# Performance work log

Hardware: AMD Instinct MI355X
Metric: run time of the kernel (lower is better)

## Reference

```python
import jax, jax.numpy as jnp
import numpy as np

B, T, D, H = 4, 2048, 1024, 16
DH = D // H
T2 = T // 2
LN_EPS = 1e-5


def setup_inputs() -> dict:
    key = jax.random.key(0)
    ks = jax.random.split(key, 10)
    x = jax.random.normal(ks[0], (B, T, D), dtype=jnp.float32)
    query = jax.random.normal(ks[1], (1, 1, D), dtype=jnp.float32) * 0.02
    s = 1.0 / np.sqrt(D)
    Wk = jax.random.uniform(ks[2], (D, D), jnp.float32, -s, s)
    Wv = jax.random.uniform(ks[3], (D, D), jnp.float32, -s, s)
    Wt = jax.random.uniform(ks[4], (D, D // 2), jnp.float32, -s, s)
    bt = jax.random.uniform(ks[5], (D // 2,), jnp.float32, -s, s)
    Wm = jax.random.uniform(ks[6], (D, 1), jnp.float32, -s, s)
    bm = jax.random.uniform(ks[7], (1,), jnp.float32, -s, s)
    ln_g = jnp.ones((D,), jnp.float32)
    ln_b = jnp.zeros((D,), jnp.float32)
    return {"x": x, "query": query, "Wk": Wk, "Wv": Wv, "Wt": Wt,
            "bt": bt, "Wm": Wm, "bm": bm, "ln_g": ln_g, "ln_b": ln_b}


def reference(x, query, Wk, Wv, Wt, bt, Wm, bm, ln_g, ln_b):
    Bx, Tx, d = x.shape
    t2 = Tx // 2
    h, dh = H, DH
    # projections -> (B, T, H, dh)
    k = (x @ Wk).reshape(Bx, Tx, h, dh)
    v = (x @ Wv).reshape(Bx, Tx, h, dh)
    q = query.reshape(h, dh)  # single learned query, shared over all coarse positions
    # scores: (B, H, T) then broadcast to (B, H, T2, T) with position-dependent mask t > 2j
    scores = jnp.einsum('hd,bthd->bht', q, k) / jnp.sqrt(jnp.asarray(dh, x.dtype))
    j_idx = jnp.arange(t2)[:, None]   # (T2, 1)
    t_idx = jnp.arange(Tx)[None, :]   # (1, T)
    mask_bias = jnp.where(t_idx > 2 * j_idx, -jnp.inf, 0.0).astype(x.dtype)  # (T2, T)
    attn = jax.nn.softmax(scores[:, :, None, :] + mask_bias[None, None], axis=-1)  # (B,H,T2,T)
    pooled = jnp.einsum('bhjt,bthd->bjhd', attn, v).reshape(Bx, t2, d)  # (B, T2, d)
    # LayerNorm over last dim
    mu = jnp.mean(pooled, axis=-1, keepdims=True)
    var = jnp.mean(jnp.square(pooled - mu), axis=-1, keepdims=True)
    pooled_n = (pooled - mu) * jax.lax.rsqrt(var + LN_EPS) * ln_g + ln_b
    theta = pooled_n @ Wt + bt                 # (B, T2, d//2)
    mag = jax.nn.sigmoid(pooled_n @ Wm + bm)   # (B, T2, 1)
    return theta, mag
```

## Files before the change

kernel.cpp:

```cpp
#include <hip/hip_runtime.h>
#include <hip/hip_bf16.h>
#include <cstdint>
#include <cstddef>

constexpr int Bc  = 4;
constexpr int Tc  = 2048;
constexpr int Dc  = 1024;
constexpr int Hc  = 16;
constexpr int DHc = 64;
constexpr int T2c = 1024;
constexpr int NCc = 32;
constexpr int NEXT = 1152;
#define LN_EPS_F 1e-5f

typedef __attribute__((ext_vector_type(8))) short bf16x8;
typedef __attribute__((ext_vector_type(8))) ushort ushort8_t;
typedef __attribute__((ext_vector_type(4))) float f32x4;

__device__ inline ushort f2bf(float f) {
    union { float f; uint32_t u; } v; v.f = f;
    uint32_t r = v.u + 0x7FFFu + ((v.u >> 16) & 1u);
    return (ushort)(r >> 16);
}
__device__ inline float bf2f(ushort u) {
    union { uint32_t u; float f; } v; v.u = ((uint32_t)u) << 16;
    return v.f;
}

__device__ inline void store_out(float v, float* p)  { *p = v; }
__device__ inline void store_out(float v, ushort* p) { *p = f2bf(v); }

__device__ inline void async_copy16(const void* g, void* lds) {
    __builtin_amdgcn_global_load_lds(
        (const __attribute__((address_space(1))) void*)g,
        (__attribute__((address_space(3))) void*)lds, 16, 0, 0);
}

constexpr int PREP_CVT  = 8192;
constexpr int PREP_WV   = PREP_CVT + 1024;
constexpr int PREP_WT   = PREP_WV + 512;
constexpr int PREP_QK   = PREP_WT + 64;
constexpr int PREP_ZERO = PREP_QK + 56;

__global__ __launch_bounds__(256) void k_prep(const float* __restrict__ x,
                                              const float* __restrict__ Wv,
                                              const float* __restrict__ Wt,
                                              const float* __restrict__ Wk,
                                              const float* __restrict__ query,
                                              ushort* __restrict__ xb,
                                              ushort* __restrict__ WvXT,
                                              ushort* __restrict__ WtT) {
    __shared__ float tile[32][33];
    int blk = blockIdx.x;
    int tid = threadIdx.x;
    if (blk < PREP_CVT) {
        int i = (blk * 256 + tid) * 4;
        float4 f = *(const float4*)(x + i);
        ushort4 o;
        o.x = f2bf(f.x); o.y = f2bf(f.y); o.z = f2bf(f.z); o.w = f2bf(f.w);
        *(ushort4*)(xb + i) = o;
    } else if (blk < PREP_WV) {
        int b2 = blk - PREP_CVT;
        int bx = b2 & 31, by = b2 >> 5;
        int tx = tid & 31, ty = tid >> 5;
        #pragma unroll
        for (int r = 0; r < 32; r += 8)
            tile[ty + r][tx] = Wv[(size_t)(by * 32 + ty + r) * Dc + bx * 32 + tx];
        __syncthreads();
        #pragma unroll
        for (int r = 0; r < 32; r += 8)
            WvXT[(size_t)(bx * 32 + ty + r) * Dc + by * 32 + tx] = f2bf(tile[tx][ty + r]);
    } else if (blk < PREP_WT) {
        int b2 = blk - PREP_WV;
        int bx = b2 & 15, by = b2 >> 4;
        int tx = tid & 31, ty = tid >> 5;
        #pragma unroll
        for (int r = 0; r < 32; r += 8)
            tile[ty + r][tx] = Wt[(size_t)(by * 32 + ty + r) * (Dc / 2) + bx * 32 + tx];
        __syncthreads();
        #pragma unroll
        for (int r = 0; r < 32; r += 8)
            WtT[(size_t)(bx * 32 + ty + r) * Dc + by * 32 + tx] = f2bf(tile[tx][ty + r]);
    } else if (blk < PREP_QK) {
        int idx = (blk - PREP_WT) * 256 + tid;
        int h = idx >> 10, i = idx & (Dc - 1);
        const float* wrow = Wk + (size_t)i * Dc + h * DHc;
        const float* qh   = query + h * DHc;
        float s = 0.f;
        #pragma unroll 8
        for (int d = 0; d < DHc; ++d) s += wrow[d] * qh[d];
        WvXT[(size_t)(Dc + h) * Dc + i] = f2bf(s * 0.125f);
    } else {
        int idx = (blk - PREP_QK) * 256 + tid;
        uint4 z = {0, 0, 0, 0};
        *(uint4*)(WvXT + (size_t)1040 * Dc + idx * 8) = z;
    }
}

__global__ __launch_bounds__(256) void k_gemm_v(const ushort* __restrict__ A,
                                                const ushort* __restrict__ Bt,
                                                ushort* __restrict__ v,
                                                float* __restrict__ scores) {
    constexpr int K = Dc;
    __shared__ ushort As[128 * 32];
    __shared__ ushort Bs[128 * 32];
    int tid = threadIdx.x;
    int wid = tid >> 6, lane = tid & 63;
    int tile_m = blockIdx.x * 128, tile_n = blockIdx.y * 128;
    int wm = wid >> 1, wn = wid & 1;

    f32x4 acc[4][4] = {};

    int lrow = lane >> 2;
    int lchunk = lane & 3;
    int quad = lane >> 4, l15 = lane & 15;

    for (int k0 = 0; k0 < K; k0 += 32) {
        #pragma unroll
        for (int r = 0; r < 2; ++r) {
            int rowgrp = wid * 2 + r;
            int row = rowgrp * 16 + lrow;
            async_copy16(A + (size_t)(tile_m + row) * K + k0 + lchunk * 8,
                         &As[rowgrp * 16 * 32]);
        }
        #pragma unroll
        for (int r = 0; r < 2; ++r) {
            int rowgrp = wid * 2 + r;
            int row = rowgrp * 16 + lrow;
            async_copy16(Bt + (size_t)(tile_n + row) * K + k0 + lchunk * 8,
                         &Bs[rowgrp * 16 * 32]);
        }
        __syncthreads();

        bf16x8 a_frag[4], b_frag[4];
        #pragma unroll
        for (int i = 0; i < 4; ++i)
            a_frag[i] = *(const bf16x8*)&As[(wm * 64 + i * 16 + l15) * 32 + quad * 8];
        #pragma unroll
        for (int j = 0; j < 4; ++j)
            b_frag[j] = *(const bf16x8*)&Bs[(wn * 64 + j * 16 + l15) * 32 + quad * 8];
        #pragma unroll
        for (int i = 0; i < 4; ++i)
            #pragma unroll
            for (int j = 0; j < 4; ++j)
                acc[i][j] = __builtin_amdgcn_mfma_f32_16x16x32_bf16(
                    a_frag[i], b_frag[j], acc[i][j], 0, 0, 0);
        __syncthreads();
    }

    #pragma unroll
    for (int j = 0; j < 4; ++j) {
        int col = tile_n + wn * 64 + j * 16 + l15;
        #pragma unroll
        for (int i = 0; i < 4; ++i) {
            #pragma unroll
            for (int r = 0; r < 4; ++r) {
                int row = tile_m + wm * 64 + i * 16 + quad * 4 + r;
                float val = acc[i][j][r];
                if (col < Dc) {
                    v[(size_t)row * Dc + col] = f2bf(val);
                } else if (col < Dc + Hc) {
                    int h = col - Dc;
                    int b = row >> 11, t = row & (Tc - 1);
                    scores[((size_t)b * Hc + h) * Tc + t] = val;
                }
            }
        }
    }
}

template <bool BIAS, typename OutT>
__global__ __launch_bounds__(256) void k_gemm_bf16(const ushort* __restrict__ A,
                                                   const ushort* __restrict__ Bt,
                                                   const float* __restrict__ bias,
                                                   OutT* __restrict__ C,
                                                   int M, int N, int K) {
    __shared__ ushort As[128 * 32];
    __shared__ ushort Bs[128 * 32];
    int tid = threadIdx.x;
    int wid = tid >> 6, lane = tid & 63;
    int tile_m = blockIdx.x * 128, tile_n = blockIdx.y * 128;
    int wm = wid >> 1, wn = wid & 1;

    f32x4 acc[4][4] = {};

    int lrow = lane >> 2;
    int lchunk = lane & 3;
    int quad = lane >> 4, l15 = lane & 15;

    for (int k0 = 0; k0 < K; k0 += 32) {
        #pragma unroll
        for (int r = 0; r < 2; ++r) {
            int rowgrp = wid * 2 + r;
            int row = rowgrp * 16 + lrow;
            async_copy16(A + (size_t)(tile_m + row) * K + k0 + lchunk * 8,
                         &As[rowgrp * 16 * 32]);
        }
        #pragma unroll
        for (int r = 0; r < 2; ++r) {
            int rowgrp = wid * 2 + r;
            int row = rowgrp * 16 + lrow;
            async_copy16(Bt + (size_t)(tile_n + row) * K + k0 + lchunk * 8,
                         &Bs[rowgrp * 16 * 32]);
        }
        __syncthreads();

        bf16x8 a_frag[4], b_frag[4];
        #pragma unroll
        for (int i = 0; i < 4; ++i)
            a_frag[i] = *(const bf16x8*)&As[(wm * 64 + i * 16 + l15) * 32 + quad * 8];
        #pragma unroll
        for (int j = 0; j < 4; ++j)
            b_frag[j] = *(const bf16x8*)&Bs[(wn * 64 + j * 16 + l15) * 32 + quad * 8];
        #pragma unroll
        for (int i = 0; i < 4; ++i)
            #pragma unroll
            for (int j = 0; j < 4; ++j)
                acc[i][j] = __builtin_amdgcn_mfma_f32_16x16x32_bf16(
                    a_frag[i], b_frag[j], acc[i][j], 0, 0, 0);
        __syncthreads();
    }

    #pragma unroll
    for (int j = 0; j < 4; ++j) {
        int col = tile_n + wn * 64 + j * 16 + l15;
        float bv = BIAS ? bias[col] : 0.f;
        #pragma unroll
        for (int i = 0; i < 4; ++i) {
            #pragma unroll
            for (int r = 0; r < 4; ++r) {
                int row = tile_m + wm * 64 + i * 16 + quad * 4 + r;
                store_out(acc[i][j][r] + bv, &C[(size_t)row * N + col]);
            }
        }
    }
}

__global__ __launch_bounds__(64) void k_chunk(const float* __restrict__ scores,
                                              const ushort* __restrict__ v,
                                              float* __restrict__ chunkL,
                                              float* __restrict__ chunkAcc) {
    int idx = blockIdx.x;
    int c = idx & (NCc - 1);
    int bh = idx / NCc;
    int h = bh & (Hc - 1), b = bh / Hc;
    int lane = threadIdx.x;
    int tgrp = lane >> 3;
    int dgrp = lane & 7;
    int t0 = c * 64;
    const float* srow = scores + (size_t)bh * Tc + t0;
    const ushort* vbase = v + ((size_t)b * Tc + t0) * Dc + h * DHc + dgrp * 8;
    float acc[8] = {};
    float lsum = 0.f;
    #pragma unroll
    for (int it = 0; it < 8; ++it) {
        int t = it * 8 + tgrp;
        float e = expf(srow[t]);
        ushort8_t vv = *(const ushort8_t*)(vbase + (size_t)t * Dc);
        #pragma unroll
        for (int k = 0; k < 8; ++k) acc[k] += e * bf2f(vv[k]);
        lsum += e;
    }
    #pragma unroll
    for (int m = 8; m < 64; m <<= 1) {
        #pragma unroll
        for (int k = 0; k < 8; ++k) acc[k] += __shfl_xor(acc[k], m);
        lsum += __shfl_xor(lsum, m);
    }
    if (tgrp == 0) {
        float4 lo = {acc[0], acc[1], acc[2], acc[3]};
        float4 hi = {acc[4], acc[5], acc[6], acc[7]};
        *(float4*)&chunkAcc[(size_t)idx * DHc + dgrp * 8]     = lo;
        *(float4*)&chunkAcc[(size_t)idx * DHc + dgrp * 8 + 4] = hi;
        if (dgrp == 0) chunkL[idx] = lsum;
    }
}

__global__ __launch_bounds__(64) void k_emit(const float* __restrict__ scores,
                                             const ushort* __restrict__ v,
                                             const float* __restrict__ chunkL,
                                             const float* __restrict__ chunkAcc,
                                             ushort* __restrict__ pooled) {
    int idx = blockIdx.x;
    int c = idx & (NCc - 1);
    int bh = idx / NCc;
    int h = bh & (Hc - 1), b = bh / Hc;
    int lane = threadIdx.x;
    int tgrp = lane >> 3, dgrp = lane & 7;
    int t0 = c * 64;
    __shared__ float E[64];
    __shared__ ushort vs[64 * DHc];
    E[lane] = expf(scores[(size_t)bh * Tc + t0 + lane]);
    const ushort* vbase = v + ((size_t)b * Tc + t0) * Dc + h * DHc + dgrp * 8;
    #pragma unroll
    for (int it = 0; it < 8; ++it) {
        int t = it * 8 + tgrp;
        *(ushort8_t*)&vs[t * DHc + dgrp * 8] = *(const ushort8_t*)(vbase + (size_t)t * Dc);
    }
    float acc = 0.f;
    for (int cc = 0; cc < c; ++cc)
        acc += chunkAcc[((size_t)bh * NCc + cc) * DHc + lane];
    float lP = (lane < c) ? chunkL[bh * NCc + lane] : 0.f;
    #pragma unroll
    for (int m = 1; m < 64; m <<= 1) lP += __shfl_xor(lP, m);
    float l = lP;
    __syncthreads();
    #pragma unroll 4
    for (int t = 0; t < 64; t += 2) {
        float e = E[t];
        acc += e * bf2f(vs[t * DHc + lane]);
        l += e;
        int j = (t0 + t) >> 1;
        pooled[((size_t)b * T2c + j) * Dc + h * DHc + lane] = f2bf(acc / l);
        float e2 = E[t + 1];
        acc += e2 * bf2f(vs[(t + 1) * DHc + lane]);
        l += e2;
    }
}

__global__ __launch_bounds__(256) void k_lnmag(const ushort* __restrict__ pooled,
                                               const float* __restrict__ g,
                                               const float* __restrict__ be,
                                               const float* __restrict__ Wm,
                                               const float* __restrict__ bm,
                                               ushort* __restrict__ out,
                                               float* __restrict__ mag) {
    int row = blockIdx.x;
    const ushort* p = pooled + (size_t)row * Dc;
    int tid = threadIdx.x;
    __shared__ float red[256];
    __shared__ float mu_s, rstd_s;
    float x4[4];
    {
        ushort4 u = *(const ushort4*)(p + tid * 4);
        x4[0] = bf2f(u.x); x4[1] = bf2f(u.y); x4[2] = bf2f(u.z); x4[3] = bf2f(u.w);
    }
    red[tid] = x4[0] + x4[1] + x4[2] + x4[3];
    __syncthreads();
    for (int off = 128; off > 0; off >>= 1) {
        if (tid < off) red[tid] += red[tid + off];
        __syncthreads();
    }
    if (tid == 0) mu_s = red[0] * (1.f / Dc);
    __syncthreads();
    float mu = mu_s;
    float vs = 0.f;
    #pragma unroll
    for (int k = 0; k < 4; ++k) { float d = x4[k] - mu; vs += d * d; }
    red[tid] = vs;
    __syncthreads();
    for (int off = 128; off > 0; off >>= 1) {
        if (tid < off) red[tid] += red[tid + off];
        __syncthreads();
    }
    if (tid == 0) rstd_s = rsqrtf(red[0] * (1.f / Dc) + LN_EPS_F);
    __syncthreads();
    float rstd = rstd_s;
    int i = tid * 4;
    float4 gv = *(const float4*)(g + i);
    float4 bv = *(const float4*)(be + i);
    float4 wv = *(const float4*)(Wm + i);
    float n0 = (x4[0] - mu) * rstd * gv.x + bv.x;
    float n1 = (x4[1] - mu) * rstd * gv.y + bv.y;
    float n2 = (x4[2] - mu) * rstd * gv.z + bv.z;
    float n3 = (x4[3] - mu) * rstd * gv.w + bv.w;
    ushort4 o;
    o.x = f2bf(n0); o.y = f2bf(n1); o.z = f2bf(n2); o.w = f2bf(n3);
    *(ushort4*)(out + (size_t)row * Dc + i) = o;
    red[tid] = bf2f(o.x) * wv.x + bf2f(o.y) * wv.y + bf2f(o.z) * wv.z + bf2f(o.w) * wv.w;
    __syncthreads();
    for (int off = 128; off > 0; off >>= 1) {
        if (tid < off) red[tid] += red[tid + off];
        __syncthreads();
    }
    if (tid == 0) {
        float z = red[0] + bm[0];
        mag[row] = 1.f / (1.f + expf(-z));
    }
}

extern "C" void kernel_launch(void* const* d_in, const int* in_sizes, int n_in,
                              void* d_out, int out_size, void* d_ws, size_t ws_size,
                              hipStream_t stream) {
    const float* x     = (const float*)d_in[0];
    const float* query = (const float*)d_in[1];
    const float* Wk    = (const float*)d_in[2];
    const float* Wv    = (const float*)d_in[3];
    const float* Wt    = (const float*)d_in[4];
    const float* bt    = (const float*)d_in[5];
    const float* Wm    = (const float*)d_in[6];
    const float* bm    = (const float*)d_in[7];
    const float* ln_g  = (const float*)d_in[8];
    const float* ln_b  = (const float*)d_in[9];
    float* out = (float*)d_out;

    char* w = (char*)d_ws;
    auto alloc = [&](size_t bytes) { char* p = w; w += (bytes + 255) & ~(size_t)255; return p; };
    ushort* v        = (ushort*)alloc((size_t)Bc * Tc * Dc * 2);
    ushort* pooled   = (ushort*)alloc((size_t)Bc * T2c * Dc * 2);
    ushort* xb       = (ushort*)alloc((size_t)Bc * Tc * Dc * 2);
    ushort* pooledn  = (ushort*)alloc((size_t)Bc * T2c * Dc * 2);
    ushort* WvXT     = (ushort*)alloc((size_t)NEXT * Dc * 2);
    ushort* WtT      = (ushort*)alloc((size_t)(Dc / 2) * Dc * 2);
    float*  scores   = (float*) alloc((size_t)Bc * Hc * Tc * 4);
    float*  chunkL   = (float*) alloc((size_t)Bc * Hc * NCc * 4);
    float*  chunkAcc = (float*) alloc((size_t)Bc * Hc * NCc * DHc * 4);

    k_prep<<<PREP_ZERO, 256, 0, stream>>>(x, Wv, Wt, Wk, query, xb, WvXT, WtT);
    k_gemm_v<<<dim3((Bc * Tc) / 128, NEXT / 128), 256, 0, stream>>>(xb, WvXT, v, scores);
    k_chunk<<<Bc * Hc * NCc, 64, 0, stream>>>(scores, v, chunkL, chunkAcc);
    k_emit<<<Bc * Hc * NCc, 64, 0, stream>>>(scores, v, chunkL, chunkAcc, pooled);
    k_lnmag<<<Bc * T2c, 256, 0, stream>>>(pooled, ln_g, ln_b, Wm, bm, pooledn,
                                          out + (size_t)Bc * T2c * (Dc / 2));
    k_gemm_bf16<true, float><<<dim3((Bc * T2c) / 128, (Dc / 2) / 128), 256, 0, stream>>>(
        pooledn, WtT, bt, out, Bc * T2c, Dc / 2, Dc);
}
```

Before: 202.4 us.

## Replace LDS-tiled GEMMs with single-wave direct-global-load 64x64 MFMA tiles

Both bf16 GEMMs drop the 256-thread, 128x128 LDS-staged tiles in favour of one 64-lane wave per 64x64 tile that loads MFMA fragments straight from global memory. The aim is to remove LDS traffic and the block barriers. The projection GEMM now launches 17 column tiles instead of 9, so the extra score columns waste only one 64-wide tile rather than most of a 128-wide one. In exchange, each wave reloads its operands from global memory with no LDS sharing and only 16-byte strided row reads, which raises L2 traffic and the reliance on cache hits.

```diff
diff --git a/kernel.cpp b/kernel.cpp
--- a/kernel.cpp
+++ b/kernel.cpp
@@ -25,15 +25,6 @@
 __device__ inline float bf2f(ushort u) {
     union { uint32_t u; float f; } v; v.u = ((uint32_t)u) << 16;
     return v.f;
-}
-
-__device__ inline void store_out(float v, float* p)  { *p = v; }
-__device__ inline void store_out(float v, ushort* p) { *p = f2bf(v); }
-
-__device__ inline void async_copy16(const void* g, void* lds) {
-    __builtin_amdgcn_global_load_lds(
-        (const __attribute__((address_space(1))) void*)g,
-        (__attribute__((address_space(3))) void*)lds, 16, 0, 0);
 }
 
 constexpr int PREP_CVT  = 8192;
@@ -97,140 +88,95 @@
     }
 }
 
-__global__ __launch_bounds__(256) void k_gemm_v(const ushort* __restrict__ A,
-                                                const ushort* __restrict__ Bt,
-                                                ushort* __restrict__ v,
-                                                float* __restrict__ scores) {
+__global__ __launch_bounds__(64) void k_gemm_v(const ushort* __restrict__ A,
+                                               const ushort* __restrict__ Bt,
+                                               ushort* __restrict__ v,
+                                               float* __restrict__ scores) {
     constexpr int K = Dc;
-    __shared__ ushort As[128 * 32];
-    __shared__ ushort Bs[128 * 32];
-    int tid = threadIdx.x;
-    int wid = tid >> 6, lane = tid & 63;
-    int tile_m = blockIdx.x * 128, tile_n = blockIdx.y * 128;
-    int wm = wid >> 1, wn = wid & 1;
+    int lane = threadIdx.x;
+    int l15 = lane & 15, quad = lane >> 4;
+    int tile_m = blockIdx.x * 64, tile_n = blockIdx.y * 64;
 
     f32x4 acc[4][4] = {};
-
-    int lrow = lane >> 2;
-    int lchunk = lane & 3;
-    int quad = lane >> 4, l15 = lane & 15;
-
+    const ushort* arow = A  + (size_t)(tile_m + l15) * K + quad * 8;
+    const ushort* brow = Bt + (size_t)(tile_n + l15) * K + quad * 8;
+
+    #pragma unroll 2
     for (int k0 = 0; k0 < K; k0 += 32) {
-        #pragma unroll
-        for (int r = 0; r < 2; ++r) {
-            int rowgrp = wid * 2 + r;
-            int row = rowgrp * 16 + lrow;
-            async_copy16(A + (size_t)(tile_m + row) * K + k0 + lchunk * 8,
-                         &As[rowgrp * 16 * 32]);
-        }
-        #pragma unroll
-        for (int r = 0; r < 2; ++r) {
-            int rowgrp = wid * 2 + r;
-            int row = rowgrp * 16 + lrow;
-            async_copy16(Bt + (size_t)(tile_n + row) * K + k0 + lchunk * 8,
-                         &Bs[rowgrp * 16 * 32]);
-        }
-        __syncthreads();
-
-        bf16x8 a_frag[4], b_frag[4];
+        bf16x8 a[4], b[4];
         #pragma unroll
         for (int i = 0; i < 4; ++i)
-            a_frag[i] = *(const bf16x8*)&As[(wm * 64 + i * 16 + l15) * 32 + quad * 8];
+            a[i] = *(const bf16x8*)(arow + (size_t)i * 16 * K + k0);
         #pragma unroll
         for (int j = 0; j < 4; ++j)
-            b_frag[j] = *(const bf16x8*)&Bs[(wn * 64 + j * 16 + l15) * 32 + quad * 8];
+            b[j] = *(const bf16x8*)(brow + (size_t)j * 16 * K + k0);
         #pragma unroll
         for (int i = 0; i < 4; ++i)
             #pragma unroll
             for (int j = 0; j < 4; ++j)
-                acc[i][j] = __builtin_amdgcn_mfma_f32_16x16x32_bf16(
-                    a_frag[i], b_frag[j], acc[i][j], 0, 0, 0);
-        __syncthreads();
+                acc[i][j] = __builtin_amdgcn_mfma_f32_16x16x32_bf16(a[i], b[j], acc[i][j], 0, 0, 0);
     }
 
     #pragma unroll
     for (int j = 0; j < 4; ++j) {
-        int col = tile_n + wn * 64 + j * 16 + l15;
+        int col = tile_n + j * 16 + l15;
         #pragma unroll
         for (int i = 0; i < 4; ++i) {
             #pragma unroll
             for (int r = 0; r < 4; ++r) {
-                int row = tile_m + wm * 64 + i * 16 + quad * 4 + r;
+                int row = tile_m + i * 16 + quad * 4 + r;
                 float val = acc[i][j][r];
                 if (col < Dc) {
                     v[(size_t)row * Dc + col] = f2bf(val);
                 } else if (col < Dc + Hc) {
                     int h = col - Dc;
-                    int b = row >> 11, t = row & (Tc - 1);
-                    scores[((size_t)b * Hc + h) * Tc + t] = val;
+                    int b2 = row >> 11, t = row & (Tc - 1);
+                    scores[((size_t)b2 * Hc + h) * Tc + t] = val;
                 }
             }
         }
     }
 }
 
-template <bool BIAS, typename OutT>
-__global__ __launch_bounds__(256) void k_gemm_bf16(const ushort* __restrict__ A,
-                                                   const ushort* __restrict__ Bt,
-                                                   const float* __restrict__ bias,
-                                                   OutT* __restrict__ C,
-                                                   int M, int N, int K) {
-    __shared__ ushort As[128 * 32];
-    __shared__ ushort Bs[128 * 32];
-    int tid = threadIdx.x;
-    int wid = tid >> 6, lane = tid & 63;
-    int tile_m = blockIdx.x * 128, tile_n = blockIdx.y * 128;
-    int wm = wid >> 1, wn = wid & 1;
+__global__ __launch_bounds__(64) void k_gemm_t(const ushort* __restrict__ A,
+                                               const ushort* __restrict__ Bt,
+                                               const float* __restrict__ bias,
+                                               float* __restrict__ C,
+                                               int N, int K) {
+    int lane = threadIdx.x;
+    int l15 = lane & 15, quad = lane >> 4;
+    int tile_m = blockIdx.x * 64, tile_n = blockIdx.y * 64;
 
     f32x4 acc[4][4] = {};
-
-    int lrow = lane >> 2;
-    int lchunk = lane & 3;
-    int quad = lane >> 4, l15 = lane & 15;
-
+    const ushort* arow = A  + (size_t)(tile_m + l15) * K + quad * 8;
+    const ushort* brow = Bt + (size_t)(tile_n + l15) * K + quad * 8;
+
+    #pragma unroll 2
     for (int k0 = 0; k0 < K; k0 += 32) {
-        #pragma unroll
-        for (int r = 0; r < 2; ++r) {
-            int rowgrp = wid * 2 + r;
-            int row = rowgrp * 16 + lrow;
-            async_copy16(A + (size_t)(tile_m + row) * K + k0 + lchunk * 8,
-                         &As[rowgrp * 16 * 32]);
-        }
-        #pragma unroll
-        for (int r = 0; r < 2; ++r) {
-            int rowgrp = wid * 2 + r;
-            int row = rowgrp * 16 + lrow;
-            async_copy16(Bt + (size_t)(tile_n + row) * K + k0 + lchunk * 8,
-                         &Bs[rowgrp * 16 * 32]);
-        }
-        __syncthreads();
-
-        bf16x8 a_frag[4], b_frag[4];
+        bf16x8 a[4], b[4];
         #pragma unroll
         for (int i = 0; i < 4; ++i)
-            a_frag[i] = *(const bf16x8*)&As[(wm * 64 + i * 16 + l15) * 32 + quad * 8];
+            a[i] = *(const bf16x8*)(arow + (size_t)i * 16 * K + k0);
         #pragma unroll
         for (int j = 0; j < 4; ++j)
-            b_frag[j] = *(const bf16x8*)&Bs[(wn * 64 + j * 16 + l15) * 32 + quad * 8];
+            b[j] = *(const bf16x8*)(brow + (size_t)j * 16 * K + k0);
         #pragma unroll
         for (int i = 0; i < 4; ++i)
             #pragma unroll
             for (int j = 0; j < 4; ++j)
-                acc[i][j] = __builtin_amdgcn_mfma_f32_16x16x32_bf16(
-                    a_frag[i], b_frag[j], acc[i][j], 0, 0, 0);
-        __syncthreads();
+                acc[i][j] = __builtin_amdgcn_mfma_f32_16x16x32_bf16(a[i], b[j], acc[i][j], 0, 0, 0);
     }
 
     #pragma unroll
     for (int j = 0; j < 4; ++j) {
-        int col = tile_n + wn * 64 + j * 16 + l15;
-        float bv = BIAS ? bias[col] : 0.f;
+        int col = tile_n + j * 16 + l15;
+        float bv = bias[col];
         #pragma unroll
         for (int i = 0; i < 4; ++i) {
             #pragma unroll
             for (int r = 0; r < 4; ++r) {
-                int row = tile_m + wm * 64 + i * 16 + quad * 4 + r;
-                store_out(acc[i][j][r] + bv, &C[(size_t)row * N + col]);
+                int row = tile_m + i * 16 + quad * 4 + r;
+                C[(size_t)row * N + col] = acc[i][j][r] + bv;
             }
         }
     }
@@ -407,11 +353,11 @@
     float*  chunkAcc = (float*) alloc((size_t)Bc * Hc * NCc * DHc * 4);
 
     k_prep<<<PREP_ZERO, 256, 0, stream>>>(x, Wv, Wt, Wk, query, xb, WvXT, WtT);
-    k_gemm_v<<<dim3((Bc * Tc) / 128, NEXT / 128), 256, 0, stream>>>(xb, WvXT, v, scores);
+    k_gemm_v<<<dim3((Bc * Tc) / 64, 17), 64, 0, stream>>>(xb, WvXT, v, scores);
     k_chunk<<<Bc * Hc * NCc, 64, 0, stream>>>(scores, v, chunkL, chunkAcc);
     k_emit<<<Bc * Hc * NCc, 64, 0, stream>>>(scores, v, chunkL, chunkAcc, pooled);
     k_lnmag<<<Bc * T2c, 256, 0, stream>>>(pooled, ln_g, ln_b, Wm, bm, pooledn,
                                           out + (size_t)Bc * T2c * (Dc / 2));
-    k_gemm_bf16<true, float><<<dim3((Bc * T2c) / 128, (Dc / 2) / 128), 256, 0, stream>>>(
-        pooledn, WtT, bt, out, Bc * T2c, Dc / 2, Dc);
-}
+    k_gemm_t<<<dim3((Bc * T2c) / 64, (Dc / 2) / 64), 64, 0, stream>>>(
+        pooledn, WtT, bt, out, Dc / 2, Dc);
+}
```

After: 245.4 us. +21.3%, slower.
